# Optimization experiments

Hardware: AMD Instinct MI355X
Metric: run time of the kernel (lower is better)

## Reference

```python
import jax, jax.numpy as jnp
import numpy as np

B, N, D, T, L = 16, 64, 4, 40, 10
H, K = 128, 4
E = N * (N - 1)


def setup_inputs() -> dict:
    key = jax.random.key(0)
    ks = jax.random.split(key, 24)
    s = 0.05
    off = np.ones((N, N)) - np.eye(N)
    recv, send = np.where(off)  # rel_rec one-hot of recv, rel_send one-hot of send
    p = {}
    p["data"] = jax.random.normal(ks[0], (B, N, D, T), jnp.float32)
    p["rel_type"] = jax.random.uniform(ks[1], (B, E, K), dtype=jnp.float32)
    p["msg_W1"] = jax.random.normal(ks[2], (K, 2 * H, H), jnp.float32) * s
    p["msg_b1"] = jnp.zeros((K, H), jnp.float32)
    p["msg_W2"] = jax.random.normal(ks[3], (K, H, H), jnp.float32) * s
    p["msg_b2"] = jnp.zeros((K, H), jnp.float32)
    p["Wr_h"] = jax.random.normal(ks[4], (H, H), jnp.float32) * s
    p["Wi_h"] = jax.random.normal(ks[5], (H, H), jnp.float32) * s
    p["Wh_h"] = jax.random.normal(ks[6], (H, H), jnp.float32) * s
    p["Wr_in"] = jax.random.normal(ks[7], (D, H), jnp.float32) * s
    p["br_in"] = jnp.zeros((H,), jnp.float32)
    p["Wi_in"] = jax.random.normal(ks[8], (D, H), jnp.float32) * s
    p["bi_in"] = jnp.zeros((H,), jnp.float32)
    p["Wn_in"] = jax.random.normal(ks[9], (D, H), jnp.float32) * s
    p["bn_in"] = jnp.zeros((H,), jnp.float32)
    p["Wo1"] = jax.random.normal(ks[10], (H, H), jnp.float32) * s
    p["bo1"] = jnp.zeros((H,), jnp.float32)
    p["Wo2"] = jax.random.normal(ks[11], (H, H), jnp.float32) * s
    p["bo2"] = jnp.zeros((H,), jnp.float32)
    p["Wo3"] = jax.random.normal(ks[12], (H, D), jnp.float32) * s
    p["bo3"] = jnp.zeros((D,), jnp.float32)
    p["recv_idx"] = jnp.asarray(recv, jnp.int32)
    p["send_idx"] = jnp.asarray(send, jnp.int32)
    return p


def _forward(data, rel_type, msg_W1, msg_b1, msg_W2, msg_b2, Wr_h, Wi_h, Wh_h,
             Wr_in, br_in, Wi_in, bi_in, Wn_in, bn_in,
             Wo1, bo1, Wo2, bo2, Wo3, bo3, recv_idx, send_idx):
    inputs = jnp.transpose(data, (0, 3, 1, 2))  # [B,T,N,D]
    Bv = inputs.shape[0]

    def single_step(ins, hidden):
        # gather == matmul with one-hot rel_send / rel_rec
        pre_msg = jnp.concatenate([hidden[:, send_idx], hidden[:, recv_idx]], axis=-1)  # [B,E,2H]
        m = jnp.tanh(jnp.einsum('bef,kfh->bkeh', pre_msg, msg_W1) + msg_b1[None, :, None, :])
        m = jnp.tanh(jnp.einsum('bkeh,khg->bkeg', m, msg_W2) + msg_b2[None, :, None, :])
        # sum over edge types weighted by rel_type, normalized by num edge types
        all_msgs = jnp.einsum('bkeh,bek->beh', m, rel_type) / K
        # scatter-add to receivers == rel_rec^T matmul; normalized by n_in_node
        agg = jnp.zeros((Bv, N, H), all_msgs.dtype).at[:, recv_idx].add(all_msgs) / D
        r = jax.nn.sigmoid(ins @ Wr_in + br_in + agg @ Wr_h)
        i = jax.nn.sigmoid(ins @ Wi_in + bi_in + agg @ Wi_h)
        n = jnp.tanh(ins @ Wn_in + bn_in + r * (agg @ Wh_h))
        hidden = (1.0 - i) * n + i * hidden
        y = jax.nn.relu(hidden @ Wo1 + bo1)
        y = jax.nn.relu(y @ Wo2 + bo2)
        pred = ins + y @ Wo3 + bo3
        return pred, hidden

    inputs_pad = jnp.concatenate([inputs, jnp.zeros((Bv, L, N, D), inputs.dtype)], axis=1)
    xs_t = jnp.transpose(inputs_pad, (1, 0, 2, 3))  # [T+L,B,N,D]

    def scan_fn(carry, xs):
        hidden, prev = carry
        step, x_t = xs
        ins = jnp.where(step < T, x_t, prev)  # burn-in then closed-loop
        pred, hidden = single_step(ins, hidden)
        return (hidden, pred), pred

    init = (jnp.zeros((Bv, N, H), jnp.float32), jnp.zeros((Bv, N, D), jnp.float32))
    _, preds = jax.lax.scan(scan_fn, init, (jnp.arange(T + L), xs_t))
    preds = jnp.transpose(preds, (1, 2, 3, 0))  # [B,N,D,T+L]
    return preds[..., -L:]


def reference(data, rel_type, msg_W1, msg_b1, msg_W2, msg_b2, Wr_h, Wi_h, Wh_h,
              Wr_in, br_in, Wi_in, bi_in, Wn_in, bn_in,
              Wo1, bo1, Wo2, bo2, Wo3, bo3, recv_idx, send_idx):
    return _forward(data, rel_type, msg_W1, msg_b1, msg_W2, msg_b2, Wr_h, Wi_h, Wh_h,
                    Wr_in, br_in, Wi_in, bi_in, Wn_in, bn_in,
                    Wo1, bo1, Wo2, bo2, Wo3, bo3, recv_idx, send_idx)
```

## Files before the change

### kernel.cpp

```cpp
#include <hip/hip_runtime.h>
#include <hip/hip_bf16.h>
#include <math.h>

#define Bb 16
#define Nn 64
#define Dd 4
#define Tt 40
#define Ll 10
#define Hh 128
#define Kk 4
#define Ee (Nn*(Nn-1))
#define BNH (Bb*Nn*Hh)
#define SIGMA 2.8853900817779268f

typedef __attribute__((ext_vector_type(8))) short short8;
typedef __attribute__((ext_vector_type(4))) float f32x4;

#define AS1 __attribute__((address_space(1)))
#define AS3 __attribute__((address_space(3)))

__device__ __forceinline__ float tanhE(float y){
    float e = __builtin_amdgcn_exp2f(y);
    float r = __builtin_amdgcn_rcpf(e + 1.0f);
    return fmaf(-2.0f, r, 1.0f);
}
__device__ __forceinline__ float tanh_fast(float x){ return tanhE(SIGMA * x); }
__device__ __forceinline__ float sigmoid_fast(float x){
    return __builtin_amdgcn_rcpf(1.0f + __expf(-x));
}
__device__ __forceinline__ unsigned short f2bf(float x){
    unsigned int u = __float_as_uint(x);
    return (unsigned short)((u + 0x7FFFu + ((u >> 16) & 1u)) >> 16);
}
__device__ __forceinline__ unsigned int pack_bf2(float lo, float hi){
    union { __hip_bfloat162 h; unsigned int u; } cv;
    cv.h = __float22bfloat162_rn(make_float2(lo, hi));
    return cv.u;
}
__device__ __forceinline__ void g2lds16(const void* g, void* l){
    __builtin_amdgcn_global_load_lds((const AS1 unsigned int*)g,
                                     (AS3 unsigned int*)l, 16, 0, 0);
}

__global__ void __launch_bounds__(256) kW2f(const float* __restrict__ W2,
                                            const float* __restrict__ b2,
                                            unsigned short* __restrict__ W2f,
                                            float* __restrict__ b2l){
    if (blockIdx.x == 32){
        int i = threadIdx.x;
        b2l[i]       = SIGMA * b2[i];
        b2l[i + 256] = SIGMA * b2[i + 256];
        return;
    }
    int t    = blockIdx.x * 256 + threadIdx.x;
    int lane = t & 63;
    int nt   = (t >> 6) & 7;
    int kc   = (t >> 9) & 3;
    int k    = (t >> 11) & 3;
    int col  = nt * 16 + (lane & 15);
    int fb   = kc * 32 + (lane >> 4) * 8;
    unsigned int w[4];
#pragma unroll
    for (int p = 0; p < 4; ++p){
        unsigned short lo = f2bf(W2[(k*Hh + fb + 2*p    )*Hh + col]);
        unsigned short hi = f2bf(W2[(k*Hh + fb + 2*p + 1)*Hh + col]);
        w[p] = (unsigned int)lo | ((unsigned int)hi << 16);
    }
    ((uint4*)W2f)[t] = make_uint4(w[0], w[1], w[2], w[3]);
}

__global__ void __launch_bounds__(256) kW1f(const float* __restrict__ W1,
                                            unsigned short* __restrict__ W1f){
    int t    = blockIdx.x * 256 + threadIdx.x;
    int lane = t & 63;
    int nt   = (t >> 6) & 7;
    int kc   = (t >> 9) & 3;
    int s    = t >> 11;
    int col  = nt * 16 + (lane & 15);
    int fb   = kc * 32 + (lane >> 4) * 8;
    unsigned int w[4];
#pragma unroll
    for (int p = 0; p < 4; ++p){
        unsigned short lo = f2bf(W1[(size_t)(s*Hh + fb + 2*p    )*Hh + col]);
        unsigned short hi = f2bf(W1[(size_t)(s*Hh + fb + 2*p + 1)*Hh + col]);
        w[p] = (unsigned int)lo | ((unsigned int)hi << 16);
    }
    ((uint4*)W1f)[t] = make_uint4(w[0], w[1], w[2], w[3]);
}

__global__ void __launch_bounds__(512, 2) kB(const unsigned short* __restrict__ hbf,
                                             const unsigned short* __restrict__ W1f,
                                             const unsigned short* __restrict__ W2f,
                                             const float* __restrict__ b1,
                                             const float* __restrict__ b2l,
                                             const float* __restrict__ rel,
                                             float* __restrict__ aggp){
    __shared__ unsigned short w2s[32*512];
    __shared__ float sfs[8192];
    __shared__ float rrs[8*Hh];
    __shared__ float rel_s[8][64];
    __shared__ float b2s[Hh];

    const int blk  = blockIdx.x;
    const int k    = blk & 3;
    const int no   = (blk >> 2) & 7;
    const int b    = blk >> 5;
    const int tid  = threadIdx.x;
    const int wave = tid >> 6;
    const int lane = tid & 63;

    {
        const uint4* src = (const uint4*)(W2f + (size_t)k*16384);
        uint4* dst = (uint4*)w2s;
#pragma unroll
        for (int i = 0; i < 4; ++i)
            g2lds16(src + tid + i*512, dst + tid + i*512);
    }
    {
        int g = tid >> 6, s = tid & 63;
        int n = no*8 + g;
        float w = 0.0f;
        if (s != n){
            int e = s - (s > n);
            w = rel[(b*Ee + n*63 + e)*Kk + k];
        }
        rel_s[g][s] = w;
    }
    if (tid < 128) b2s[tid] = b2l[k*Hh + tid];

    const short8* hv = (const short8*)hbf;
    const short8* wv = (const short8*)W1f;
    const int colb  = lane & 15;
    const int rbase = (lane >> 4) << 2;

    {
        const int mt  = wave >> 1;
        const int nt0 = (wave & 1) * 4;
        short8 a[4];
#pragma unroll
        for (int kc = 0; kc < 4; ++kc)
            a[kc] = hv[((size_t)((b*4 + mt)*4) + kc)*64 + lane];
        f32x4 acc[4];
#pragma unroll
        for (int j = 0; j < 4; ++j) acc[j] = (f32x4)0.0f;
#pragma unroll
        for (int kc = 0; kc < 4; ++kc){
#pragma unroll
            for (int j = 0; j < 4; ++j){
                short8 bf = wv[((size_t)((2*k)*4 + kc)*8 + nt0 + j)*64 + lane];
                acc[j] = __builtin_amdgcn_mfma_f32_16x16x32_bf16(a[kc], bf, acc[j], 0, 0, 0);
            }
        }
        char* sfsB = (char*)sfs;
#pragma unroll
        for (int j = 0; j < 4; ++j){
            int h  = (nt0 + j)*16 + colb;
            int fg = h >> 3, fl = h & 7;
            int sw = (fg & 7) << 4;
#pragma unroll
            for (int r = 0; r < 4; ++r){
                int node = mt*16 + rbase + r;
                int A = fg*2048 + node*32 + fl*4;
                *(float*)(sfsB + (A ^ sw)) = SIGMA * acc[j][r];
            }
        }
    }
    {
        const int mtr = no >> 1;
        short8 a[4];
#pragma unroll
        for (int kc = 0; kc < 4; ++kc)
            a[kc] = hv[((size_t)((b*4 + mtr)*4) + kc)*64 + lane];
        f32x4 acc = (f32x4)0.0f;
#pragma unroll
        for (int kc = 0; kc < 4; ++kc){
            short8 bf = wv[((size_t)((2*k+1)*4 + kc)*8 + wave)*64 + lane];
            acc = __builtin_amdgcn_mfma_f32_16x16x32_bf16(a[kc], bf, acc, 0, 0, 0);
        }
        const int h   = wave*16 + colb;
        const float b1v = b1[k*Hh + h];
        const int lo  = (no & 1) * 8;
#pragma unroll
        for (int r = 0; r < 4; ++r){
            int row = rbase + r;
            if (row >= lo && row < lo + 8)
                rrs[(row - lo)*Hh + h] = SIGMA * (acc[r] + b1v);
        }
    }
    __syncthreads();

    const int n    = no*8 + wave;
    const int fo   = lane >> 4;
    const int srow = lane & 15;
    const char* sfsB = (const char*)sfs;
    const float* rrw = rrs + wave*Hh;
    const short8* w2v = (const short8*)w2s;
    const float* relw = rel_s[wave];

    float aggacc[8];
#pragma unroll
    for (int nt = 0; nt < 8; ++nt) aggacc[nt] = 0.0f;

#pragma unroll 1
    for (int st = 0; st < 4; ++st){
        short8 a[4];
#pragma unroll
        for (int kc = 0; kc < 4; ++kc){
            const int fg = kc*4 + fo;
            const int A  = fg*2048 + (st*16 + srow)*32;
            const int sw = (fg & 7) << 4;
            float4 s0 = *(const float4*)(sfsB + (A ^ sw));
            float4 s1 = *(const float4*)(sfsB + ((A + 16) ^ sw));
            const float4* rp = (const float4*)(rrw + fg*8);
            float4 r0 = rp[0], r1 = rp[1];
            union { short8 v; unsigned int u[4]; } av;
            av.u[0] = pack_bf2(tanhE(s0.x+r0.x), tanhE(s0.y+r0.y));
            av.u[1] = pack_bf2(tanhE(s0.z+r0.z), tanhE(s0.w+r0.w));
            av.u[2] = pack_bf2(tanhE(s1.x+r1.x), tanhE(s1.y+r1.y));
            av.u[3] = pack_bf2(tanhE(s1.z+r1.z), tanhE(s1.w+r1.w));
            a[kc] = av.v;
        }

        f32x4 acc[8];
#pragma unroll
        for (int nt = 0; nt < 8; ++nt) acc[nt] = (f32x4)0.0f;
#pragma unroll
        for (int kc = 0; kc < 4; ++kc){
#pragma unroll
            for (int nt = 0; nt < 8; ++nt){
                short8 bfr = w2v[(kc*8 + nt)*64 + lane];
                acc[nt] = __builtin_amdgcn_mfma_f32_16x16x32_bf16(a[kc], bfr, acc[nt], 0, 0, 0);
            }
        }

#pragma unroll
        for (int nt = 0; nt < 8; ++nt){
            float bv = b2s[nt*16 + colb];
            float s = 0.0f;
#pragma unroll
            for (int r = 0; r < 4; ++r)
                s = fmaf(relw[st*16 + rbase + r], tanhE(fmaf(SIGMA, acc[nt][r], bv)), s);
            s += __shfl_xor(s, 16);
            s += __shfl_xor(s, 32);
            aggacc[nt] += s;
        }
    }

    if (lane < 16){
#pragma unroll
        for (int nt = 0; nt < 8; ++nt)
            aggp[(size_t)k*BNH + (size_t)(b*64 + n)*Hh + nt*16 + lane] = aggacc[nt];
    }
}

__global__ void __launch_bounds__(256) kC(const float* __restrict__ data,
                                          const float* __restrict__ aggp,
                                          float* __restrict__ hidden,
                                          float* __restrict__ prevpred,
                                          unsigned short* __restrict__ hbf,
                                          const float* __restrict__ Wr_in, const float* __restrict__ br_in,
                                          const float* __restrict__ Wi_in, const float* __restrict__ bi_in,
                                          const float* __restrict__ Wn_in, const float* __restrict__ bn_in,
                                          const float* __restrict__ Wr_h,  const float* __restrict__ Wi_h,
                                          const float* __restrict__ Wh_h,
                                          const float* __restrict__ Wo1,   const float* __restrict__ bo1,
                                          const float* __restrict__ Wo2,   const float* __restrict__ bo2,
                                          const float* __restrict__ Wo3,   const float* __restrict__ bo3,
                                          float* __restrict__ out, int t){
    __shared__ float aggL[4][Hh];
    __shared__ float buf[4][Hh];
    __shared__ float insL[4][Dd];
    __shared__ float psh[3][4][Hh];

    const int bn0 = blockIdx.x * 4;
    const int tid = threadIdx.x;
    const int h   = tid & 127;
    const int fh  = tid >> 7;
    const int f0  = fh * 64;

    for (int s2 = tid; s2 < 512; s2 += 256){
        int g = s2 >> 7, hx = s2 & 127;
        int bn = bn0 + g;
        aggL[g][hx] = (aggp[bn*Hh + hx] + aggp[BNH + bn*Hh + hx] +
                       aggp[2*BNH + bn*Hh + hx] + aggp[3*BNH + bn*Hh + hx]) * (1.0f/16.0f);
    }
    if (tid < 16){
        int g = tid >> 2, d = tid & 3;
        int bn = bn0 + g;
        insL[g][d] = (t < Tt) ? data[(bn*Dd + d)*Tt + t] : prevpred[bn*Dd + d];
    }
    __syncthreads();

    float rh[4] = {0,0,0,0}, ih[4] = {0,0,0,0}, hh[4] = {0,0,0,0};
    for (int f = f0; f < f0 + 64; ++f){
        float wr = Wr_h[f*Hh + h], wi = Wi_h[f*Hh + h], wh = Wh_h[f*Hh + h];
#pragma unroll
        for (int g = 0; g < 4; ++g){
            float av = aggL[g][f];
            rh[g] += av*wr; ih[g] += av*wi; hh[g] += av*wh;
        }
    }
    if (fh){
#pragma unroll
        for (int g = 0; g < 4; ++g){
            psh[0][g][h] = rh[g]; psh[1][g][h] = ih[g]; psh[2][g][h] = hh[g];
        }
    }
    __syncthreads();

    if (!fh){
        const float wr0 = Wr_in[h],        wr1 = Wr_in[Hh + h],
                    wr2 = Wr_in[2*Hh + h], wr3 = Wr_in[3*Hh + h];
        const float wi0 = Wi_in[h],        wi1 = Wi_in[Hh + h],
                    wi2 = Wi_in[2*Hh + h], wi3 = Wi_in[3*Hh + h];
        const float wn0 = Wn_in[h],        wn1 = Wn_in[Hh + h],
                    wn2 = Wn_in[2*Hh + h], wn3 = Wn_in[3*Hh + h];
        const float brv = br_in[h], biv = bi_in[h], bnv = bn_in[h];
        const int kc  = h >> 5;
        const int lhi = (h >> 3) & 3;
        const int j   = h & 7;
#pragma unroll
        for (int g = 0; g < 4; ++g){
            float i0 = insL[g][0], i1 = insL[g][1], i2 = insL[g][2], i3 = insL[g][3];
            float r  = sigmoid_fast(brv + i0*wr0 + i1*wr1 + i2*wr2 + i3*wr3 + rh[g] + psh[0][g][h]);
            float ii = sigmoid_fast(biv + i0*wi0 + i1*wi1 + i2*wi2 + i3*wi3 + ih[g] + psh[1][g][h]);
            float nn = tanh_fast   (bnv + i0*wn0 + i1*wn1 + i2*wn2 + i3*wn3 + r*(hh[g] + psh[2][g][h]));
            float hold = hidden[(bn0+g)*Hh + h];
            float hnew = (1.0f - ii)*nn + ii*hold;
            hidden[(bn0+g)*Hh + h] = hnew;
            buf[g][h] = hnew;
            int bn   = bn0 + g;
            int bb   = bn >> 6, node64 = bn & 63;
            int Mt   = node64 >> 4;
            int lane = (node64 & 15) + lhi*16;
            hbf[((size_t)((bb*4 + Mt)*4 + kc)*64 + lane)*8 + j] = f2bf(hnew);
        }
    }
    __syncthreads();

    {
        float yp[4] = {0,0,0,0};
        for (int f = f0; f < f0 + 64; ++f){
            float wv1 = Wo1[f*Hh + h];
#pragma unroll
            for (int g = 0; g < 4; ++g) yp[g] += buf[g][f]*wv1;
        }
        if (fh){
#pragma unroll
            for (int g = 0; g < 4; ++g) psh[0][g][h] = yp[g];
        }
        __syncthreads();
        if (!fh){
            float b1v = bo1[h];
#pragma unroll
            for (int g = 0; g < 4; ++g) buf[g][h] = fmaxf(b1v + yp[g] + psh[0][g][h], 0.0f);
        }
    }
    __syncthreads();

    {
        float yp[4] = {0,0,0,0};
        for (int f = f0; f < f0 + 64; ++f){
            float wv2 = Wo2[f*Hh + h];
#pragma unroll
            for (int g = 0; g < 4; ++g) yp[g] += buf[g][f]*wv2;
        }
        if (fh){
#pragma unroll
            for (int g = 0; g < 4; ++g) psh[0][g][h] = yp[g];
        }
        __syncthreads();
        if (!fh){
            float b2v = bo2[h];
#pragma unroll
            for (int g = 0; g < 4; ++g) buf[g][h] = fmaxf(b2v + yp[g] + psh[0][g][h], 0.0f);
        }
    }
    __syncthreads();

    if (tid < 16){
        int g = tid >> 2, d = tid & 3;
        float pv = bo3[d];
        for (int f = 0; f < Hh; ++f) pv += buf[g][f]*Wo3[f*Dd + d];
        pv += insL[g][d];
        int bn = bn0 + g;
        prevpred[bn*Dd + d] = pv;
        if (t >= Tt) out[(bn*Dd + d)*Ll + (t - Tt)] = pv;
    }
}

extern "C" void kernel_launch(void* const* d_in, const int* in_sizes, int n_in,
                              void* d_out, int out_size, void* d_ws, size_t ws_size,
                              hipStream_t stream){
    const float* data  = (const float*)d_in[0];
    const float* rel   = (const float*)d_in[1];
    const float* W1    = (const float*)d_in[2];
    const float* b1    = (const float*)d_in[3];
    const float* W2    = (const float*)d_in[4];
    const float* b2    = (const float*)d_in[5];
    const float* Wr_h  = (const float*)d_in[6];
    const float* Wi_h  = (const float*)d_in[7];
    const float* Wh_h  = (const float*)d_in[8];
    const float* Wr_in = (const float*)d_in[9];
    const float* br_in = (const float*)d_in[10];
    const float* Wi_in = (const float*)d_in[11];
    const float* bi_in = (const float*)d_in[12];
    const float* Wn_in = (const float*)d_in[13];
    const float* bn_in = (const float*)d_in[14];
    const float* Wo1   = (const float*)d_in[15];
    const float* bo1   = (const float*)d_in[16];
    const float* Wo2   = (const float*)d_in[17];
    const float* bo2   = (const float*)d_in[18];
    const float* Wo3   = (const float*)d_in[19];
    const float* bo3   = (const float*)d_in[20];

    float* out = (float*)d_out;
    float* ws  = (float*)d_ws;

    float* hidden   = ws;
    float* prevpred = hidden + BNH;
    unsigned short* hbf = (unsigned short*)(prevpred + Bb*Nn*Dd);
    float* aggp     = (float*)(hbf + BNH);
    unsigned short* W2f = (unsigned short*)(aggp + 4*BNH);
    float* b2l      = (float*)(W2f + 65536);
    unsigned short* W1f = (unsigned short*)(b2l + 512);

    hipMemsetAsync(hidden, 0, (size_t)(Bb*Nn*Hh + Bb*Nn*Dd)*4 + (size_t)BNH*2, stream);
    kW2f<<<33, 256, 0, stream>>>(W2, b2, W2f, b2l);
    kW1f<<<64, 256, 0, stream>>>(W1, W1f);

    for (int t = 0; t < Tt + Ll; ++t){
        kB<<<512, 512, 0, stream>>>(hbf, W1f, W2f, b1, b2l, rel, aggp);
        kC<<<256, 256, 0, stream>>>(data, aggp, hidden, prevpred, hbf,
                                    Wr_in, br_in, Wi_in, bi_in, Wn_in, bn_in,
                                    Wr_h, Wi_h, Wh_h,
                                    Wo1, bo1, Wo2, bo2, Wo3, bo3, out, t);
    }
}
```

Measured before the change: 2.174 ms.

## Halve kC rows per block, interleave aggp by k, remap kB block order

```diff
diff --git a/kernel.cpp b/kernel.cpp
--- a/kernel.cpp
+++ b/kernel.cpp
@@ -102,9 +102,10 @@
     __shared__ float b2s[Hh];
 
     const int blk  = blockIdx.x;
-    const int k    = blk & 3;
-    const int no   = (blk >> 2) & 7;
-    const int b    = blk >> 5;
+    const int k    = blk >> 7;
+    const int rem  = blk & 127;
+    const int b    = rem >> 3;
+    const int no   = rem & 7;
     const int tid  = threadIdx.x;
     const int wave = tid >> 6;
     const int lane = tid & 63;
@@ -247,9 +248,10 @@
     }
 
     if (lane < 16){
+        const int bn = b*64 + n;
 #pragma unroll
         for (int nt = 0; nt < 8; ++nt)
-            aggp[(size_t)k*BNH + (size_t)(b*64 + n)*Hh + nt*16 + lane] = aggacc[nt];
+            aggp[((size_t)bn*4 + k)*Hh + nt*16 + lane] = aggacc[nt];
     }
 }
 
@@ -267,42 +269,47 @@
                                           const float* __restrict__ Wo2,   const float* __restrict__ bo2,
                                           const float* __restrict__ Wo3,   const float* __restrict__ bo3,
                                           float* __restrict__ out, int t){
-    __shared__ float aggL[4][Hh];
-    __shared__ float buf[4][Hh];
-    __shared__ float insL[4][Dd];
-    __shared__ float psh[3][4][Hh];
-
-    const int bn0 = blockIdx.x * 4;
+    __shared__ float aggL[2][Hh];
+    __shared__ float buf[2][Hh];
+    __shared__ float insL[2][Dd];
+    __shared__ float psh[3][2][Hh];
+
+    const int p   = blockIdx.x;
+    const int no  = p & 7;
+    const int m   = p >> 3;
+    const int b   = m >> 2;
+    const int j   = (m & 3) + no*4;
+    const int bn0 = b*64 + j*2;
+
     const int tid = threadIdx.x;
     const int h   = tid & 127;
     const int fh  = tid >> 7;
     const int f0  = fh * 64;
 
-    for (int s2 = tid; s2 < 512; s2 += 256){
-        int g = s2 >> 7, hx = s2 & 127;
-        int bn = bn0 + g;
-        aggL[g][hx] = (aggp[bn*Hh + hx] + aggp[BNH + bn*Hh + hx] +
-                       aggp[2*BNH + bn*Hh + hx] + aggp[3*BNH + bn*Hh + hx]) * (1.0f/16.0f);
-    }
-    if (tid < 16){
+    {
+        int g = fh;
+        const float* ap = aggp + ((size_t)(bn0 + g)*4)*Hh + h;
+        aggL[g][h] = (ap[0] + ap[Hh] + ap[2*Hh] + ap[3*Hh]) * (1.0f/16.0f);
+    }
+    if (tid < 8){
         int g = tid >> 2, d = tid & 3;
         int bn = bn0 + g;
         insL[g][d] = (t < Tt) ? data[(bn*Dd + d)*Tt + t] : prevpred[bn*Dd + d];
     }
     __syncthreads();
 
-    float rh[4] = {0,0,0,0}, ih[4] = {0,0,0,0}, hh[4] = {0,0,0,0};
+    float rh[2] = {0,0}, ih[2] = {0,0}, hh[2] = {0,0};
     for (int f = f0; f < f0 + 64; ++f){
         float wr = Wr_h[f*Hh + h], wi = Wi_h[f*Hh + h], wh = Wh_h[f*Hh + h];
 #pragma unroll
-        for (int g = 0; g < 4; ++g){
+        for (int g = 0; g < 2; ++g){
             float av = aggL[g][f];
             rh[g] += av*wr; ih[g] += av*wi; hh[g] += av*wh;
         }
     }
     if (fh){
 #pragma unroll
-        for (int g = 0; g < 4; ++g){
+        for (int g = 0; g < 2; ++g){
             psh[0][g][h] = rh[g]; psh[1][g][h] = ih[g]; psh[2][g][h] = hh[g];
         }
     }
@@ -318,9 +325,9 @@
         const float brv = br_in[h], biv = bi_in[h], bnv = bn_in[h];
         const int kc  = h >> 5;
         const int lhi = (h >> 3) & 3;
-        const int j   = h & 7;
-#pragma unroll
-        for (int g = 0; g < 4; ++g){
+        const int jj  = h & 7;
+#pragma unroll
+        for (int g = 0; g < 2; ++g){
             float i0 = insL[g][0], i1 = insL[g][1], i2 = insL[g][2], i3 = insL[g][3];
             float r  = sigmoid_fast(brv + i0*wr0 + i1*wr1 + i2*wr2 + i3*wr3 + rh[g] + psh[0][g][h]);
             float ii = sigmoid_fast(biv + i0*wi0 + i1*wi1 + i2*wi2 + i3*wi3 + ih[g] + psh[1][g][h]);
@@ -333,52 +340,52 @@
             int bb   = bn >> 6, node64 = bn & 63;
             int Mt   = node64 >> 4;
             int lane = (node64 & 15) + lhi*16;
-            hbf[((size_t)((bb*4 + Mt)*4 + kc)*64 + lane)*8 + j] = f2bf(hnew);
-        }
-    }
-    __syncthreads();
-
-    {
-        float yp[4] = {0,0,0,0};
+            hbf[((size_t)((bb*4 + Mt)*4 + kc)*64 + lane)*8 + jj] = f2bf(hnew);
+        }
+    }
+    __syncthreads();
+
+    {
+        float yp[2] = {0,0};
         for (int f = f0; f < f0 + 64; ++f){
             float wv1 = Wo1[f*Hh + h];
 #pragma unroll
-            for (int g = 0; g < 4; ++g) yp[g] += buf[g][f]*wv1;
+            for (int g = 0; g < 2; ++g) yp[g] += buf[g][f]*wv1;
         }
         if (fh){
 #pragma unroll
-            for (int g = 0; g < 4; ++g) psh[0][g][h] = yp[g];
+            for (int g = 0; g < 2; ++g) psh[0][g][h] = yp[g];
         }
         __syncthreads();
         if (!fh){
             float b1v = bo1[h];
 #pragma unroll
-            for (int g = 0; g < 4; ++g) buf[g][h] = fmaxf(b1v + yp[g] + psh[0][g][h], 0.0f);
-        }
-    }
-    __syncthreads();
-
-    {
-        float yp[4] = {0,0,0,0};
+            for (int g = 0; g < 2; ++g) buf[g][h] = fmaxf(b1v + yp[g] + psh[0][g][h], 0.0f);
+        }
+    }
+    __syncthreads();
+
+    {
+        float yp[2] = {0,0};
         for (int f = f0; f < f0 + 64; ++f){
             float wv2 = Wo2[f*Hh + h];
 #pragma unroll
-            for (int g = 0; g < 4; ++g) yp[g] += buf[g][f]*wv2;
+            for (int g = 0; g < 2; ++g) yp[g] += buf[g][f]*wv2;
         }
         if (fh){
 #pragma unroll
-            for (int g = 0; g < 4; ++g) psh[0][g][h] = yp[g];
+            for (int g = 0; g < 2; ++g) psh[0][g][h] = yp[g];
         }
         __syncthreads();
         if (!fh){
             float b2v = bo2[h];
 #pragma unroll
-            for (int g = 0; g < 4; ++g) buf[g][h] = fmaxf(b2v + yp[g] + psh[0][g][h], 0.0f);
-        }
-    }
-    __syncthreads();
-
-    if (tid < 16){
+            for (int g = 0; g < 2; ++g) buf[g][h] = fmaxf(b2v + yp[g] + psh[0][g][h], 0.0f);
+        }
+    }
+    __syncthreads();
+
+    if (tid < 8){
         int g = tid >> 2, d = tid & 3;
         float pv = bo3[d];
         for (int f = 0; f < Hh; ++f) pv += buf[g][f]*Wo3[f*Dd + d];
@@ -431,7 +438,7 @@
 
     for (int t = 0; t < Tt + Ll; ++t){
         kB<<<512, 512, 0, stream>>>(hbf, W1f, W2f, b1, b2l, rel, aggp);
-        kC<<<256, 256, 0, stream>>>(data, aggp, hidden, prevpred, hbf,
+        kC<<<512, 256, 0, stream>>>(data, aggp, hidden, prevpred, hbf,
                                     Wr_in, br_in, Wi_in, bi_in, Wn_in, bn_in,
                                     Wr_h, Wi_h, Wh_h,
                                     Wo1, bo1, Wo2, bo2, Wo3, bo3, out, t);
```

Result: faster. 1.948 ms, median of 2 (-10.4%).
